# Performance work log

Measured on AMD Instinct MI355X. Metric: run time of the kernel, lower is better.

## Reference

```python
import jax, jax.numpy as jnp
import numpy as np

N_NODES = 50000
N_EDGES = 800000
IN_DIM = 256
OUT_DIM = 256


def setup_inputs() -> dict:
    key = jax.random.key(0)
    k1, k2, k3, k4, k5, k6 = jax.random.split(key, 6)
    x = jax.random.normal(k1, (N_NODES, IN_DIM), dtype=jnp.float32)
    adj_rows = jax.random.randint(k2, (N_EDGES,), 0, N_NODES)
    adj_cols = jax.random.randint(k3, (N_EDGES,), 0, N_NODES)
    adj_vals = jax.random.uniform(k4, (N_EDGES,), dtype=jnp.float32)
    stdv = 1.0 / np.sqrt(OUT_DIM)
    W = jax.random.uniform(k5, (IN_DIM, OUT_DIM), minval=-stdv, maxval=stdv, dtype=jnp.float32)
    b = jax.random.uniform(k6, (OUT_DIM,), minval=-stdv, maxval=stdv, dtype=jnp.float32)
    return {"x": x, "adj_rows": adj_rows, "adj_cols": adj_cols, "adj_vals": adj_vals, "W": W, "b": b}


def reference(x, adj_rows, adj_cols, adj_vals, W, b):
    # hidden = x @ W  (first sparse.mm; x treated dense, identical math)
    hidden = jnp.matmul(x, W)  # [N, out_dim]
    # output = adj @ hidden via COO SpMM: gather source rows, scale, scatter-add to dest rows
    msgs = adj_vals[:, None] * hidden[adj_cols]  # [E, out_dim]
    output = jax.ops.segment_sum(msgs, adj_rows, num_segments=N_NODES)  # [N, out_dim]
    return output + b
```

## Files before the change

### kernel.cpp

```cpp
#include <hip/hip_runtime.h>

#define N_NODES 50000
#define N_EDGES 800000
#define DIM     256
#define N_STRIPS 3125

typedef __attribute__((ext_vector_type(8))) short bf16x8;
typedef __attribute__((ext_vector_type(4))) float f32x4;

__device__ __forceinline__ unsigned short f2bf(float f) {
    unsigned u = __float_as_uint(f);
    unsigned r = (u + 0x7fffu + ((u >> 16) & 1u)) >> 16;
    return (unsigned short)r;
}
__device__ __forceinline__ float bf2f(unsigned short h) {
    return __uint_as_float((unsigned)h << 16);
}

__global__ __launch_bounds__(256)
void wtrans(const float* __restrict__ W, unsigned short* __restrict__ Wt) {
    const int n = blockIdx.x;
    const int k = threadIdx.x;
    Wt[n * DIM + k] = f2bf(W[(size_t)k * DIM + n]);
}

__global__ __launch_bounds__(512, 2)
void gemm_mfma(const float* __restrict__ X, const unsigned short* __restrict__ Wt,
               unsigned short* __restrict__ Hb) {
    __shared__ unsigned short wl[DIM * DIM];
    const int tid = threadIdx.x;

    {
        const uint4* src = (const uint4*)Wt;
#pragma unroll
        for (int i = 0; i < 16; ++i) {
            const int c   = i * 512 + tid;
            const int row = c >> 5;
            const int kb  = (c & 31) * 16;
            const int dst = row * 512 + (kb ^ ((row & 7) << 4));
            *(uint4*)((char*)wl + dst) = src[c];
        }
    }
    __syncthreads();

    const int wid   = tid >> 6;
    const int lane  = tid & 63;
    const int strip = blockIdx.x * 8 + wid;
    if (strip >= N_STRIPS) return;

    const int r0   = strip * 16;
    const int arow = lane & 15;
    const int kgrp = lane >> 4;
    const float* xrow = X + (size_t)(r0 + arow) * DIM + kgrp * 8;

    float4 araw[8][2];
#pragma unroll
    for (int ks = 0; ks < 8; ++ks) {
        araw[ks][0] = *(const float4*)(xrow + ks * 32);
        araw[ks][1] = *(const float4*)(xrow + ks * 32 + 4);
    }

    f32x4 acc[16];
#pragma unroll
    for (int nt = 0; nt < 16; ++nt) acc[nt] = f32x4{0.f, 0.f, 0.f, 0.f};

    const int swz = (arow & 7) << 4;
#pragma unroll
    for (int ks = 0; ks < 8; ++ks) {
        bf16x8 a;
        a[0] = (short)f2bf(araw[ks][0].x); a[1] = (short)f2bf(araw[ks][0].y);
        a[2] = (short)f2bf(araw[ks][0].z); a[3] = (short)f2bf(araw[ks][0].w);
        a[4] = (short)f2bf(araw[ks][1].x); a[5] = (short)f2bf(araw[ks][1].y);
        a[6] = (short)f2bf(araw[ks][1].z); a[7] = (short)f2bf(araw[ks][1].w);
        const int kb = ((ks * 32 + kgrp * 8) * 2) ^ swz;
#pragma unroll
        for (int nt = 0; nt < 16; ++nt) {
            const int n = nt * 16 + arow;
            const bf16x8 b = *(const bf16x8*)((const char*)wl + n * 512 + kb);
            acc[nt] = __builtin_amdgcn_mfma_f32_16x16x32_bf16(a, b, acc[nt], 0, 0, 0);
        }
    }

    const int crow0 = r0 + kgrp * 4;
#pragma unroll
    for (int nt = 0; nt < 16; ++nt) {
#pragma unroll
        for (int q = 0; q < 4; ++q) {
            Hb[(size_t)(crow0 + q) * DIM + nt * 16 + arow] = f2bf(acc[nt][q]);
        }
    }
}

__global__ __launch_bounds__(256)
void zero_aux(int* __restrict__ cnt, int* __restrict__ cursor) {
    const int i = blockIdx.x * 256 + threadIdx.x;
    if (i < N_NODES) { cnt[i] = 0; cursor[i] = 0; }
}

__global__ __launch_bounds__(256)
void count_edges(const int* __restrict__ rows, int* __restrict__ cnt) {
    const int e = blockIdx.x * 256 + threadIdx.x;
    if (e < N_EDGES) atomicAdd(&cnt[rows[e]], 1);
}

__device__ __forceinline__ int block_excl_scan_256(int v, int* wsum, int* total) {
    const int lane = threadIdx.x & 63;
    const int wave = threadIdx.x >> 6;
    int x = v;
#pragma unroll
    for (int off = 1; off < 64; off <<= 1) {
        const int y = __shfl_up(x, off, 64);
        if (lane >= off) x += y;
    }
    if (lane == 63) wsum[wave] = x;
    __syncthreads();
    if (threadIdx.x == 0) {
        int s = 0;
#pragma unroll
        for (int w = 0; w < 4; ++w) { const int t = wsum[w]; wsum[w] = s; s += t; }
        *total = s;
    }
    __syncthreads();
    return wsum[wave] + x - v;
}

__global__ __launch_bounds__(256)
void scan_blocks(const int* __restrict__ cnt, int* __restrict__ offs,
                 int* __restrict__ bsum) {
    __shared__ int wsum[4];
    __shared__ int total;
    const int i = blockIdx.x * 256 + threadIdx.x;
    const int v = (i < N_NODES) ? cnt[i] : 0;
    const int excl = block_excl_scan_256(v, wsum, &total);
    if (i < N_NODES) offs[i] = excl;
    if (threadIdx.x == 0) bsum[blockIdx.x] = total;
}

#define NBLK_NODES 196

__global__ __launch_bounds__(256)
void scan_top(int* __restrict__ bsum) {
    __shared__ int wsum[4];
    __shared__ int total;
    const int t = threadIdx.x;
    const int v = (t < NBLK_NODES) ? bsum[t] : 0;
    const int excl = block_excl_scan_256(v, wsum, &total);
    if (t < NBLK_NODES) bsum[t] = excl;
}

__global__ __launch_bounds__(256)
void scan_add(int* __restrict__ offs, const int* __restrict__ bsum) {
    const int i = blockIdx.x * 256 + threadIdx.x;
    if (i < N_NODES) offs[i] += bsum[blockIdx.x];
    if (i == 0) offs[N_NODES] = N_EDGES;
}

__global__ __launch_bounds__(256)
void fill_edges(const int* __restrict__ rows, const int* __restrict__ cols,
                const float* __restrict__ vals, const int* __restrict__ offs,
                int* __restrict__ cursor, int2* __restrict__ pe) {
    const int e = blockIdx.x * 256 + threadIdx.x;
    if (e >= N_EDGES) return;
    const int r = rows[e];
    const int p = atomicAdd(&cursor[r], 1);
    pe[offs[r] + p] = make_int2(cols[e], __float_as_int(vals[e]));
}

__global__ __launch_bounds__(256)
void spmm(const unsigned short* __restrict__ Hb, const int* __restrict__ offs,
          const int2* __restrict__ pe, const float* __restrict__ bias,
          float* __restrict__ out) {
    const int row  = blockIdx.x * 4 + (threadIdx.x >> 6);
    const int lane = threadIdx.x & 63;
    if (row >= N_NODES) return;
    const int beg = offs[row];
    const int end = offs[row + 1];
    float4 acc = make_float4(0.f, 0.f, 0.f, 0.f);
    int i = beg;
    for (; i + 3 < end; i += 4) {
        const int2 e0 = pe[i], e1 = pe[i+1], e2 = pe[i+2], e3 = pe[i+3];
        const ushort4 h0 = *(const ushort4*)&Hb[(size_t)e0.x * DIM + lane * 4];
        const ushort4 h1 = *(const ushort4*)&Hb[(size_t)e1.x * DIM + lane * 4];
        const ushort4 h2 = *(const ushort4*)&Hb[(size_t)e2.x * DIM + lane * 4];
        const ushort4 h3 = *(const ushort4*)&Hb[(size_t)e3.x * DIM + lane * 4];
        const float v0 = __int_as_float(e0.y), v1 = __int_as_float(e1.y);
        const float v2 = __int_as_float(e2.y), v3 = __int_as_float(e3.y);
        acc.x += v0 * bf2f(h0.x) + v1 * bf2f(h1.x) + v2 * bf2f(h2.x) + v3 * bf2f(h3.x);
        acc.y += v0 * bf2f(h0.y) + v1 * bf2f(h1.y) + v2 * bf2f(h2.y) + v3 * bf2f(h3.y);
        acc.z += v0 * bf2f(h0.z) + v1 * bf2f(h1.z) + v2 * bf2f(h2.z) + v3 * bf2f(h3.z);
        acc.w += v0 * bf2f(h0.w) + v1 * bf2f(h1.w) + v2 * bf2f(h2.w) + v3 * bf2f(h3.w);
    }
    for (; i < end; ++i) {
        const int2 e0 = pe[i];
        const ushort4 h0 = *(const ushort4*)&Hb[(size_t)e0.x * DIM + lane * 4];
        const float v0 = __int_as_float(e0.y);
        acc.x += v0 * bf2f(h0.x);
        acc.y += v0 * bf2f(h0.y);
        acc.z += v0 * bf2f(h0.z);
        acc.w += v0 * bf2f(h0.w);
    }
    const float4 bb = *(const float4*)&bias[lane * 4];
    acc.x += bb.x; acc.y += bb.y; acc.z += bb.z; acc.w += bb.w;
    *(float4*)&out[(size_t)row * DIM + lane * 4] = acc;
}

extern "C" void kernel_launch(void* const* d_in, const int* in_sizes, int n_in,
                              void* d_out, int out_size, void* d_ws, size_t ws_size,
                              hipStream_t stream) {
    const float* x        = (const float*)d_in[0];
    const int*   adj_rows = (const int*)d_in[1];
    const int*   adj_cols = (const int*)d_in[2];
    const float* adj_vals = (const float*)d_in[3];
    const float* W        = (const float*)d_in[4];
    const float* b        = (const float*)d_in[5];
    float*       out      = (float*)d_out;

    char* ws = (char*)d_ws;
    size_t off = 0;
    auto alloc = [&](size_t bytes) {
        void* p = ws + off;
        off = (off + bytes + 255) & ~(size_t)255;
        return p;
    };
    unsigned short* hiddenb = (unsigned short*)alloc((size_t)N_NODES * DIM * sizeof(unsigned short));
    unsigned short* Wt      = (unsigned short*)alloc((size_t)DIM * DIM * sizeof(unsigned short));
    int*   offs   = (int*)  alloc((N_NODES + 1) * sizeof(int));
    int*   cnt    = (int*)  alloc(N_NODES * sizeof(int));
    int*   cursor = (int*)  alloc(N_NODES * sizeof(int));
    int*   bsum   = (int*)  alloc(256 * sizeof(int));
    int2*  pe     = (int2*) alloc((size_t)N_EDGES * sizeof(int2));

    wtrans<<<DIM, 256, 0, stream>>>(W, Wt);

    gemm_mfma<<<(N_STRIPS + 7) / 8, 512, 0, stream>>>(x, Wt, hiddenb);

    zero_aux<<<NBLK_NODES, 256, 0, stream>>>(cnt, cursor);
    count_edges<<<(N_EDGES + 255) / 256, 256, 0, stream>>>(adj_rows, cnt);
    scan_blocks<<<NBLK_NODES, 256, 0, stream>>>(cnt, offs, bsum);
    scan_top<<<1, 256, 0, stream>>>(bsum);
    scan_add<<<NBLK_NODES, 256, 0, stream>>>(offs, bsum);
    fill_edges<<<(N_EDGES + 255) / 256, 256, 0, stream>>>(
        adj_rows, adj_cols, adj_vals, offs, cursor, pe);

    spmm<<<(N_NODES + 3) / 4, 256, 0, stream>>>(hiddenb, offs, pe, b, out);
}
```

Baseline: 266.5 us.

## Process 32-row strips in GEMM, deepen SpMM unroll, memset aux counters

Each GEMM wave now computes two 16-row tiles, so every LDS read of W feeds two MFMAs, and the X loads for the next k-step are issued one step early. The SpMM inner loop is unrolled to 8 edges with 32-bit index math to keep more gathers in flight. The zero_aux kernel is replaced by a single hipMemsetAsync over a merged count/cursor buffer. The changes cost more registers for two accumulator sets, which may lower occupancy, and they halve the number of GEMM waves.

```diff
diff --git a/kernel.cpp b/kernel.cpp
--- a/kernel.cpp
+++ b/kernel.cpp
@@ -3,7 +3,7 @@
 #define N_NODES 50000
 #define N_EDGES 800000
 #define DIM     256
-#define N_STRIPS 3125
+#define STRIPS32 1563
 
 typedef __attribute__((ext_vector_type(8))) short bf16x8;
 typedef __attribute__((ext_vector_type(4))) float f32x4;
@@ -29,7 +29,6 @@
                unsigned short* __restrict__ Hb) {
     __shared__ unsigned short wl[DIM * DIM];
     const int tid = threadIdx.x;
-
     {
         const uint4* src = (const uint4*)Wt;
 #pragma unroll
@@ -46,55 +45,69 @@
     const int wid   = tid >> 6;
     const int lane  = tid & 63;
     const int strip = blockIdx.x * 8 + wid;
-    if (strip >= N_STRIPS) return;
-
-    const int r0   = strip * 16;
+    if (strip >= STRIPS32) return;
+
+    const int r0   = strip * 32;
     const int arow = lane & 15;
     const int kgrp = lane >> 4;
-    const float* xrow = X + (size_t)(r0 + arow) * DIM + kgrp * 8;
-
-    float4 araw[8][2];
+    const int ra = r0 + arow;
+    const int rb = r0 + 16 + arow;
+    const float* xa = X + (size_t)(ra < N_NODES ? ra : N_NODES - 1) * DIM + kgrp * 8;
+    const float* xb = X + (size_t)(rb < N_NODES ? rb : N_NODES - 1) * DIM + kgrp * 8;
+
+    f32x4 acc[2][16];
+#pragma unroll
+    for (int h = 0; h < 2; ++h)
+#pragma unroll
+        for (int nt = 0; nt < 16; ++nt) acc[h][nt] = f32x4{0.f, 0.f, 0.f, 0.f};
+
+    const int swz = (arow & 7) << 4;
+
+    float4 pa0 = *(const float4*)(xa);
+    float4 pa1 = *(const float4*)(xa + 4);
+    float4 pb0 = *(const float4*)(xb);
+    float4 pb1 = *(const float4*)(xb + 4);
+
 #pragma unroll
     for (int ks = 0; ks < 8; ++ks) {
-        araw[ks][0] = *(const float4*)(xrow + ks * 32);
-        araw[ks][1] = *(const float4*)(xrow + ks * 32 + 4);
-    }
-
-    f32x4 acc[16];
-#pragma unroll
-    for (int nt = 0; nt < 16; ++nt) acc[nt] = f32x4{0.f, 0.f, 0.f, 0.f};
-
-    const int swz = (arow & 7) << 4;
-#pragma unroll
-    for (int ks = 0; ks < 8; ++ks) {
-        bf16x8 a;
-        a[0] = (short)f2bf(araw[ks][0].x); a[1] = (short)f2bf(araw[ks][0].y);
-        a[2] = (short)f2bf(araw[ks][0].z); a[3] = (short)f2bf(araw[ks][0].w);
-        a[4] = (short)f2bf(araw[ks][1].x); a[5] = (short)f2bf(araw[ks][1].y);
-        a[6] = (short)f2bf(araw[ks][1].z); a[7] = (short)f2bf(araw[ks][1].w);
+        bf16x8 a0, a1;
+        a0[0] = (short)f2bf(pa0.x); a0[1] = (short)f2bf(pa0.y);
+        a0[2] = (short)f2bf(pa0.z); a0[3] = (short)f2bf(pa0.w);
+        a0[4] = (short)f2bf(pa1.x); a0[5] = (short)f2bf(pa1.y);
+        a0[6] = (short)f2bf(pa1.z); a0[7] = (short)f2bf(pa1.w);
+        a1[0] = (short)f2bf(pb0.x); a1[1] = (short)f2bf(pb0.y);
+        a1[2] = (short)f2bf(pb0.z); a1[3] = (short)f2bf(pb0.w);
+        a1[4] = (short)f2bf(pb1.x); a1[5] = (short)f2bf(pb1.y);
+        a1[6] = (short)f2bf(pb1.z); a1[7] = (short)f2bf(pb1.w);
+        if (ks < 7) {
+            pa0 = *(const float4*)(xa + (ks + 1) * 32);
+            pa1 = *(const float4*)(xa + (ks + 1) * 32 + 4);
+            pb0 = *(const float4*)(xb + (ks + 1) * 32);
+            pb1 = *(const float4*)(xb + (ks + 1) * 32 + 4);
+        }
         const int kb = ((ks * 32 + kgrp * 8) * 2) ^ swz;
 #pragma unroll
         for (int nt = 0; nt < 16; ++nt) {
             const int n = nt * 16 + arow;
             const bf16x8 b = *(const bf16x8*)((const char*)wl + n * 512 + kb);
-            acc[nt] = __builtin_amdgcn_mfma_f32_16x16x32_bf16(a, b, acc[nt], 0, 0, 0);
-        }
-    }
-
-    const int crow0 = r0 + kgrp * 4;
-#pragma unroll
-    for (int nt = 0; nt < 16; ++nt) {
-#pragma unroll
-        for (int q = 0; q < 4; ++q) {
-            Hb[(size_t)(crow0 + q) * DIM + nt * 16 + arow] = f2bf(acc[nt][q]);
-        }
-    }
-}
-
-__global__ __launch_bounds__(256)
-void zero_aux(int* __restrict__ cnt, int* __restrict__ cursor) {
-    const int i = blockIdx.x * 256 + threadIdx.x;
-    if (i < N_NODES) { cnt[i] = 0; cursor[i] = 0; }
+            acc[0][nt] = __builtin_amdgcn_mfma_f32_16x16x32_bf16(a0, b, acc[0][nt], 0, 0, 0);
+            acc[1][nt] = __builtin_amdgcn_mfma_f32_16x16x32_bf16(a1, b, acc[1][nt], 0, 0, 0);
+        }
+    }
+
+#pragma unroll
+    for (int h = 0; h < 2; ++h) {
+        const int crow0 = r0 + h * 16 + kgrp * 4;
+#pragma unroll
+        for (int nt = 0; nt < 16; ++nt) {
+#pragma unroll
+            for (int q = 0; q < 4; ++q) {
+                const int r = crow0 + q;
+                if (r < N_NODES)
+                    Hb[(size_t)r * DIM + nt * 16 + arow] = f2bf(acc[h][nt][q]);
+            }
+        }
+    }
 }
 
 __global__ __launch_bounds__(256)
@@ -175,24 +188,29 @@
     if (row >= N_NODES) return;
     const int beg = offs[row];
     const int end = offs[row + 1];
+    const unsigned lb = (unsigned)lane * 4;
     float4 acc = make_float4(0.f, 0.f, 0.f, 0.f);
     int i = beg;
-    for (; i + 3 < end; i += 4) {
-        const int2 e0 = pe[i], e1 = pe[i+1], e2 = pe[i+2], e3 = pe[i+3];
-        const ushort4 h0 = *(const ushort4*)&Hb[(size_t)e0.x * DIM + lane * 4];
-        const ushort4 h1 = *(const ushort4*)&Hb[(size_t)e1.x * DIM + lane * 4];
-        const ushort4 h2 = *(const ushort4*)&Hb[(size_t)e2.x * DIM + lane * 4];
-        const ushort4 h3 = *(const ushort4*)&Hb[(size_t)e3.x * DIM + lane * 4];
-        const float v0 = __int_as_float(e0.y), v1 = __int_as_float(e1.y);
-        const float v2 = __int_as_float(e2.y), v3 = __int_as_float(e3.y);
-        acc.x += v0 * bf2f(h0.x) + v1 * bf2f(h1.x) + v2 * bf2f(h2.x) + v3 * bf2f(h3.x);
-        acc.y += v0 * bf2f(h0.y) + v1 * bf2f(h1.y) + v2 * bf2f(h2.y) + v3 * bf2f(h3.y);
-        acc.z += v0 * bf2f(h0.z) + v1 * bf2f(h1.z) + v2 * bf2f(h2.z) + v3 * bf2f(h3.z);
-        acc.w += v0 * bf2f(h0.w) + v1 * bf2f(h1.w) + v2 * bf2f(h2.w) + v3 * bf2f(h3.w);
+    for (; i + 8 <= end; i += 8) {
+        int2 e[8];
+#pragma unroll
+        for (int j = 0; j < 8; ++j) e[j] = pe[i + j];
+        ushort4 h[8];
+#pragma unroll
+        for (int j = 0; j < 8; ++j)
+            h[j] = *(const ushort4*)&Hb[((unsigned)e[j].x << 8) + lb];
+#pragma unroll
+        for (int j = 0; j < 8; ++j) {
+            const float v = __int_as_float(e[j].y);
+            acc.x += v * bf2f(h[j].x);
+            acc.y += v * bf2f(h[j].y);
+            acc.z += v * bf2f(h[j].z);
+            acc.w += v * bf2f(h[j].w);
+        }
     }
     for (; i < end; ++i) {
         const int2 e0 = pe[i];
-        const ushort4 h0 = *(const ushort4*)&Hb[(size_t)e0.x * DIM + lane * 4];
+        const ushort4 h0 = *(const ushort4*)&Hb[((unsigned)e0.x << 8) + lb];
         const float v0 = __int_as_float(e0.y);
         acc.x += v0 * bf2f(h0.x);
         acc.y += v0 * bf2f(h0.y);
@@ -224,17 +242,18 @@
     };
     unsigned short* hiddenb = (unsigned short*)alloc((size_t)N_NODES * DIM * sizeof(unsigned short));
     unsigned short* Wt      = (unsigned short*)alloc((size_t)DIM * DIM * sizeof(unsigned short));
-    int*   offs   = (int*)  alloc((N_NODES + 1) * sizeof(int));
-    int*   cnt    = (int*)  alloc(N_NODES * sizeof(int));
-    int*   cursor = (int*)  alloc(N_NODES * sizeof(int));
-    int*   bsum   = (int*)  alloc(256 * sizeof(int));
-    int2*  pe     = (int2*) alloc((size_t)N_EDGES * sizeof(int2));
+    int*   offs    = (int*)  alloc((N_NODES + 1) * sizeof(int));
+    int*   cntcur  = (int*)  alloc((size_t)2 * N_NODES * sizeof(int));
+    int*   bsum    = (int*)  alloc(256 * sizeof(int));
+    int2*  pe      = (int2*) alloc((size_t)N_EDGES * sizeof(int2));
+    int* cnt    = cntcur;
+    int* cursor = cntcur + N_NODES;
 
     wtrans<<<DIM, 256, 0, stream>>>(W, Wt);
 
-    gemm_mfma<<<(N_STRIPS + 7) / 8, 512, 0, stream>>>(x, Wt, hiddenb);
-
-    zero_aux<<<NBLK_NODES, 256, 0, stream>>>(cnt, cursor);
+    gemm_mfma<<<(STRIPS32 + 7) / 8, 512, 0, stream>>>(x, Wt, hiddenb);
+
+    hipMemsetAsync(cntcur, 0, (size_t)2 * N_NODES * sizeof(int), stream);
     count_edges<<<(N_EDGES + 255) / 256, 256, 0, stream>>>(adj_rows, cnt);
     scan_blocks<<<NBLK_NODES, 256, 0, stream>>>(cnt, offs, bsum);
     scan_top<<<1, 256, 0, stream>>>(bsum);
```

After: 264.9 us. Within noise of the previous version (-0.6%).
